# Kernel tuning notes

Measured on AMD Instinct MI355X. Metric: run time of the kernel, lower is better.

The kernel has to match this reference:

```python
import jax, jax.numpy as jnp
import numpy as np

B, DIMS = 8192, 1024
FCN = [DIMS, 2048, 1024, 512, 1]   # self.fcn_dims = [dims] + fcn_dims + [1]
C = 8                               # cluster_num
NLAYERS = len(FCN) - 1              # layer_num = 4


def setup_inputs() -> dict:
    key = jax.random.key(0)
    ks = jax.random.split(key, 2 + 2 * NLAYERS)
    inp = {}
    inp["x"] = jax.random.normal(ks[0], (B, DIMS), dtype=jnp.float32)
    # cluster centers, L2-normalized rows (as in __init__)
    c = jax.random.normal(ks[1], (C, DIMS), dtype=jnp.float32)
    inp["center"] = c / jnp.linalg.norm(c, axis=1, keepdims=True)
    for i in range(NLAYERS):
        fan_in, fan_out = FCN[i], FCN[i + 1]
        # xavier_uniform with relu gain
        gain = float(np.sqrt(2.0))
        bound = gain * float(np.sqrt(6.0 / (fan_in + fan_out)))
        inp[f"w0_{i}"] = jax.random.uniform(ks[2 + 2 * i], (fan_in, fan_out), jnp.float32, -bound, bound)
        inp[f"wc_{i}"] = jax.random.uniform(ks[3 + 2 * i], (C, fan_in, fan_out), jnp.float32, -bound, bound)
    return inp


def _forward(x, center, w0s, wcs):
    # --- router (eval mode: single pass, no center update, no grad) ---
    xd = jax.lax.stop_gradient(x)
    sij = xd @ jax.lax.stop_gradient(center).T          # [B, C]
    router = jnp.argmax(sij, axis=1)                     # [B]
    # --- all cluster towers, gated weights w0 * w_d ---
    h = jnp.broadcast_to(x[None], (C,) + x.shape)        # [C, B, dims]
    for i in range(NLAYERS - 1):
        w = w0s[i][None] * wcs[i]                        # [C, in, out]
        h = jax.nn.relu(jnp.einsum('cbi,cio->cbo', h, w))
    w = w0s[-1][None] * wcs[-1]                          # [C, in, 1]
    h = jax.nn.sigmoid(jnp.einsum('cbi,cio->cbo', h, w))  # [C, B, 1]
    out = jnp.transpose(h[:, :, 0])                      # [B, C]
    # gather per-sample selected cluster output
    return jnp.take_along_axis(out, router[:, None], axis=1)[:, 0]  # [B]


def reference(x, center, w0_0, w0_1, w0_2, w0_3, wc_0, wc_1, wc_2, wc_3):
    w0s = [w0_0, w0_1, w0_2, w0_3]
    wcs = [wc_0, wc_1, wc_2, wc_3]
    return _forward(x, center, w0s, wcs)
```

## Files before the change

kernel.cpp:

```cpp
#include <hip/hip_runtime.h>
#include <hip/hip_bf16.h>

#define B_SZ 8192
#define DIMS 1024
#define CLN 8
#define BM 128
#define PADMAX (B_SZ + CLN * BM)
#define MAX_TILES (B_SZ / BM + CLN)

typedef __attribute__((ext_vector_type(8))) __bf16 bf16x8;
typedef __attribute__((ext_vector_type(8))) short short8;
typedef __attribute__((ext_vector_type(4))) short short4v;
typedef __attribute__((ext_vector_type(4))) float f32x4;

__device__ __forceinline__ short f2bf(float f) {
  __hip_bfloat16 h = __float2bfloat16(f);
  return __builtin_bit_cast(short, h);
}
__device__ __forceinline__ float bf2f(short s) {
  unsigned u = ((unsigned)(unsigned short)s) << 16;
  return __builtin_bit_cast(float, u);
}

__device__ __forceinline__ void gl_lds16(const short* g, short* l) {
  __builtin_amdgcn_global_load_lds(
      (const __attribute__((address_space(1))) unsigned int*)(unsigned long long)(uintptr_t)g,
      (__attribute__((address_space(3))) unsigned int*)(unsigned long long)(uintptr_t)l,
      16, 0, 0);
}

__global__ void router_kernel(const float* __restrict__ x, const float* __restrict__ center,
                              int* __restrict__ router, short* __restrict__ xb) {
  const int tid = threadIdx.x;
  const int lane = tid & 63;
  const int w = tid >> 6;
  const int s = blockIdx.x * 4 + w;
  const float4* xr = (const float4*)(x + (size_t)s * DIMS);
  float4 xv[4];
#pragma unroll
  for (int j = 0; j < 4; ++j) xv[j] = xr[j * 64 + lane];
  if (xb) {
    short* xbr = xb + (size_t)s * DIMS;
#pragma unroll
    for (int j = 0; j < 4; ++j) {
      short4v sv;
      sv[0] = f2bf(xv[j].x); sv[1] = f2bf(xv[j].y);
      sv[2] = f2bf(xv[j].z); sv[3] = f2bf(xv[j].w);
      *(short4v*)(xbr + j * 256 + lane * 4) = sv;
    }
  }
  float p[CLN];
#pragma unroll
  for (int c = 0; c < CLN; ++c) {
    const float4* cr = (const float4*)(center + (size_t)c * DIMS);
    float acc = 0.f;
#pragma unroll
    for (int j = 0; j < 4; ++j) {
      float4 cv = cr[j * 64 + lane];
      acc += xv[j].x * cv.x + xv[j].y * cv.y + xv[j].z * cv.z + xv[j].w * cv.w;
    }
    p[c] = acc;
  }
#pragma unroll
  for (int c = 0; c < CLN; ++c) {
#pragma unroll
    for (int m = 1; m < 64; m <<= 1) p[c] += __shfl_xor(p[c], m);
  }
  if (lane == 0) {
    int best = 0; float bv = p[0];
#pragma unroll
    for (int c = 1; c < CLN; ++c) { if (p[c] > bv) { bv = p[c]; best = c; } }
    router[s] = best;
  }
}

__global__ void sort_kernel(const int* __restrict__ router, int* __restrict__ counts,
                            int* __restrict__ pstart, int* __restrict__ meta,
                            int* __restrict__ tile_c, int* __restrict__ tile_r,
                            int* __restrict__ order) {
  __shared__ int bins[CLN];
  __shared__ int cur[CLN];
  __shared__ int ps_s[CLN + 1];
  const int t = threadIdx.x;
  const int lane = t & 63;
  if (t < CLN) bins[t] = 0;
  __syncthreads();
  int myc[8];
#pragma unroll
  for (int j = 0; j < 8; ++j) myc[j] = router[t + 1024 * j];
#pragma unroll
  for (int j = 0; j < 8; ++j) {
#pragma unroll
    for (int c = 0; c < CLN; ++c) {
      unsigned long long m = __ballot(myc[j] == c);
      if (lane == 0 && m) atomicAdd(&bins[c], __popcll(m));
    }
  }
  __syncthreads();
  if (t == 0) {
    int ps = 0, nt = 0;
    for (int c = 0; c < CLN; ++c) {
      const int tot = bins[c];
      counts[c] = tot; pstart[c] = ps; ps_s[c] = ps; cur[c] = 0;
      const int tiles = (tot + BM - 1) / BM;
      for (int i = 0; i < tiles; ++i) { tile_c[nt] = c; tile_r[nt] = ps + i * BM; ++nt; }
      ps += tiles * BM;
    }
    pstart[CLN] = ps; ps_s[CLN] = ps; meta[0] = nt; meta[1] = ps;
  }
  __syncthreads();
#pragma unroll
  for (int j = 0; j < 8; ++j) {
    const int s = t + 1024 * j;
    const int c = myc[j];
    int pos = 0;
#pragma unroll
    for (int cc = 0; cc < CLN; ++cc) {
      unsigned long long m = __ballot(c == cc);
      int b = 0;
      if (lane == 0 && m) b = atomicAdd(&cur[cc], __popcll(m));
      b = __shfl(b, 0);
      if (c == cc) pos = ps_s[cc] + b + __popcll(m & ((1ull << lane) - 1ull));
    }
    order[pos] = s;
  }
  __syncthreads();
  for (int p = t; p < PADMAX; p += 1024) {
#pragma unroll
    for (int c = 0; c < CLN; ++c) {
      if (p >= ps_s[c] && p < ps_s[c + 1]) {
        if (p - ps_s[c] >= bins[c]) order[p] = order[ps_s[c]];
        break;
      }
    }
  }
}

template <int K, int N>
__device__ __forceinline__ void gate_body(const float* __restrict__ w0,
                                          const float* __restrict__ wc,
                                          short* __restrict__ gwt, int bx, short* t) {
  constexpr int NK = K / 32, NN = N / 64;
  const int c = bx / (NK * NN);
  const int rem = bx % (NK * NN);
  const int k0 = (rem % NK) * 32;
  const int n0 = (rem / NK) * 64;
  const int tid = threadIdx.x;
  const int lk = tid >> 4;
  const int ln = (tid & 15) * 4;
  const float* w0p = w0 + (size_t)k0 * N + n0;
  const float* wcp = wc + (size_t)c * K * N + (size_t)k0 * N + n0;
#pragma unroll
  for (int i = 0; i < 2; ++i) {
    const int k = lk + i * 16;
    float4 a = *(const float4*)(w0p + (size_t)k * N + ln);
    float4 b = *(const float4*)(wcp + (size_t)k * N + ln);
    short* d = &t[k * 65 + ln];
    d[0] = f2bf(a.x * b.x); d[1] = f2bf(a.y * b.y);
    d[2] = f2bf(a.z * b.z); d[3] = f2bf(a.w * b.w);
  }
  __syncthreads();
  const int wn = tid >> 2;
  const int wk = (tid & 3) * 8;
  short8 v;
#pragma unroll
  for (int j = 0; j < 8; ++j) v[j] = t[(wk + j) * 65 + wn];
  *(short8*)(gwt + ((size_t)c * N + n0 + wn) * K + k0 + wk) = v;
}

__global__ void gate_all(const float* __restrict__ w00, const float* __restrict__ wc0, short* g0,
                         const float* __restrict__ w01, const float* __restrict__ wc1, short* g1,
                         const float* __restrict__ w02, const float* __restrict__ wc2, short* g2) {
  __shared__ short t[32 * 65];
  const int bx = blockIdx.x;
  if (bx < 8192)       gate_body<1024, 2048>(w00, wc0, g0, bx, t);
  else if (bx < 16384) gate_body<2048, 1024>(w01, wc1, g1, bx - 8192, t);
  else                 gate_body<1024, 512>(w02, wc2, g2, bx - 16384, t);
}

template <int K, int N>
__global__ void gate_kernel(const float* __restrict__ w0, const float* __restrict__ wc,
                            short* __restrict__ gwt) {
  __shared__ short t[32 * 65];
  gate_body<K, N>(w0, wc, gwt, blockIdx.x, t);
}

template <int K, int N, bool GATHER>
__global__ void gemm_async(const short* __restrict__ Abase, const short* __restrict__ gwt,
                           short* __restrict__ Aout, const int* __restrict__ order,
                           const int* __restrict__ tile_c, const int* __restrict__ tile_r,
                           const int* __restrict__ meta) {
  constexpr int NT = N / 128;
  const int bt = blockIdx.x / NT;
  if (bt >= meta[0]) return;
  const int n0 = (blockIdx.x % NT) * 128;
  const int cl = tile_c[bt];
  const int row0 = tile_r[bt];

  __shared__ __align__(16) short As0[128 * 32];
  __shared__ __align__(16) short As1[128 * 32];
  __shared__ __align__(16) short Bs0[128 * 32];
  __shared__ __align__(16) short Bs1[128 * 32];

  const int tid = threadIdx.x;
  const int lane = tid & 63;
  const int w = tid >> 6;
  const int wm = w >> 1;
  const int wn = w & 1;

  const int lrow = lane >> 2;
  const int kofs = (lane & 3) << 3;
  const short* ga0;
  const short* ga1;
  if (GATHER) {
    ga0 = Abase + (size_t)order[row0 + w * 16 + lrow] * K + kofs;
    ga1 = Abase + (size_t)order[row0 + 64 + w * 16 + lrow] * K + kofs;
  } else {
    ga0 = Abase + (size_t)(row0 + w * 16 + lrow) * K + kofs;
    ga1 = ga0 + (size_t)64 * K;
  }
  const short* gb0 = gwt + ((size_t)cl * N + n0 + w * 16 + lrow) * K + kofs;
  const short* gb1 = gb0 + (size_t)64 * K;
  short* lo = (short*)((char*)nullptr);
  (void)lo;
  short* lA0a = &As0[w * 16 * 32];
  short* lA0b = &As0[(64 + w * 16) * 32];
  short* lA1a = &As1[w * 16 * 32];
  short* lA1b = &As1[(64 + w * 16) * 32];
  short* lB0a = &Bs0[w * 16 * 32];
  short* lB0b = &Bs0[(64 + w * 16) * 32];
  short* lB1a = &Bs1[w * 16 * 32];
  short* lB1b = &Bs1[(64 + w * 16) * 32];

  f32x4 acc[4][4] = {};
  const int arL = wm * 64 + (lane & 15);
  const int bcL = wn * 64 + (lane & 15);
  const int kq = (lane >> 4) << 3;

  for (int kb = 0; kb < K; kb += 64) {
    __syncthreads();
    gl_lds16(ga0 + kb, lA0a);
    gl_lds16(ga1 + kb, lA0b);
    gl_lds16(ga0 + kb + 32, lA1a);
    gl_lds16(ga1 + kb + 32, lA1b);
    gl_lds16(gb0 + kb, lB0a);
    gl_lds16(gb1 + kb, lB0b);
    gl_lds16(gb0 + kb + 32, lB1a);
    gl_lds16(gb1 + kb + 32, lB1b);
    __syncthreads();

#pragma unroll
    for (int h = 0; h < 2; ++h) {
      const short* Ap = h ? As1 : As0;
      const short* Bp = h ? Bs1 : Bs0;
      short8 af[4], bfr[4];
#pragma unroll
      for (int mi = 0; mi < 4; ++mi) af[mi] = *(const short8*)&Ap[(arL + mi * 16) * 32 + kq];
#pragma unroll
      for (int ni = 0; ni < 4; ++ni) bfr[ni] = *(const short8*)&Bp[(bcL + ni * 16) * 32 + kq];
#pragma unroll
      for (int mi = 0; mi < 4; ++mi) {
#pragma unroll
        for (int ni = 0; ni < 4; ++ni) {
          acc[mi][ni] = __builtin_amdgcn_mfma_f32_16x16x32_bf16(
              __builtin_bit_cast(bf16x8, af[mi]), __builtin_bit_cast(bf16x8, bfr[ni]),
              acc[mi][ni], 0, 0, 0);
        }
      }
    }
  }

  const int er = (lane >> 4) << 2;
  const int ec = lane & 15;
#pragma unroll
  for (int mi = 0; mi < 4; ++mi) {
#pragma unroll
    for (int ni = 0; ni < 4; ++ni) {
#pragma unroll
      for (int r = 0; r < 4; ++r) {
        float vv = fmaxf(acc[mi][ni][r], 0.f);
        const int row = row0 + wm * 64 + mi * 16 + er + r;
        const int col = n0 + wn * 64 + ni * 16 + ec;
        Aout[(size_t)row * N + col] = f2bf(vv);
      }
    }
  }
}

template <int K, int N, bool GATHER>
__global__ void gemm_layer(const float* __restrict__ Xf, const short* __restrict__ Ain,
                           const float* __restrict__ w0, const float* __restrict__ wc,
                           short* __restrict__ Aout,
                           const int* __restrict__ order,
                           const int* __restrict__ tile_c, const int* __restrict__ tile_r,
                           const int* __restrict__ meta) {
  const int bt = blockIdx.x;
  if (bt >= meta[0]) return;
  const int cl = tile_c[bt];
  const int row0 = tile_r[bt];
  const int n0 = blockIdx.y * 128;

  __shared__ __align__(16) short As[128 * 40];
  __shared__ __align__(16) short Bs[128 * 40];

  const int tid = threadIdx.x;
  const int lane = tid & 63;
  const int wm = (tid >> 6) >> 1;
  const int wn = (tid >> 6) & 1;

  f32x4 acc[4][4] = {};

  const int arow = tid >> 2;
  const int akseg = (tid & 3) << 3;
  const int bn = tid & 127;
  const int bkq = (tid >> 7) << 3;

  const float* xr0 = nullptr; const float* xr1 = nullptr;
  const short* ar0 = nullptr; const short* ar1 = nullptr;
  if (GATHER) {
    xr0 = Xf + (size_t)order[row0 + arow] * K + akseg;
    xr1 = Xf + (size_t)order[row0 + arow + 64] * K + akseg;
  } else {
    ar0 = Ain + (size_t)(row0 + arow) * K + akseg;
    ar1 = Ain + (size_t)(row0 + arow + 64) * K + akseg;
  }
  const float* w0p = w0 + n0 + bn;
  const float* wcp = wc + (size_t)cl * K * N + n0 + bn;

  for (int kb = 0; kb < K; kb += 32) {
    __syncthreads();
    if (GATHER) {
      float4 a = *(const float4*)(xr0 + kb);
      float4 b = *(const float4*)(xr0 + kb + 4);
      short8 v;
      v[0] = f2bf(a.x); v[1] = f2bf(a.y); v[2] = f2bf(a.z); v[3] = f2bf(a.w);
      v[4] = f2bf(b.x); v[5] = f2bf(b.y); v[6] = f2bf(b.z); v[7] = f2bf(b.w);
      *(short8*)&As[arow * 40 + akseg] = v;
      a = *(const float4*)(xr1 + kb);
      b = *(const float4*)(xr1 + kb + 4);
      v[0] = f2bf(a.x); v[1] = f2bf(a.y); v[2] = f2bf(a.z); v[3] = f2bf(a.w);
      v[4] = f2bf(b.x); v[5] = f2bf(b.y); v[6] = f2bf(b.z); v[7] = f2bf(b.w);
      *(short8*)&As[(arow + 64) * 40 + akseg] = v;
    } else {
      *(short8*)&As[arow * 40 + akseg] = *(const short8*)(ar0 + kb);
      *(short8*)&As[(arow + 64) * 40 + akseg] = *(const short8*)(ar1 + kb);
    }
#pragma unroll
    for (int half = 0; half < 2; ++half) {
      const int kk = bkq + half * 16;
      short8 v;
#pragma unroll
      for (int j = 0; j < 8; ++j) {
        const size_t off = (size_t)(kb + kk + j) * N;
        v[j] = f2bf(w0p[off] * wcp[off]);
      }
      *(short8*)&Bs[bn * 40 + kk] = v;
    }
    __syncthreads();

    const int arL = wm * 64 + (lane & 15);
    const int kq = (lane >> 4) << 3;
    const int bcL = wn * 64 + (lane & 15);
    short8 af[4], bfr[4];
#pragma unroll
    for (int mi = 0; mi < 4; ++mi) af[mi] = *(const short8*)&As[(arL + mi * 16) * 40 + kq];
#pragma unroll
    for (int ni = 0; ni < 4; ++ni) bfr[ni] = *(const short8*)&Bs[(bcL + ni * 16) * 40 + kq];
#pragma unroll
    for (int mi = 0; mi < 4; ++mi) {
#pragma unroll
      for (int ni = 0; ni < 4; ++ni) {
        acc[mi][ni] = __builtin_amdgcn_mfma_f32_16x16x32_bf16(
            __builtin_bit_cast(bf16x8, af[mi]), __builtin_bit_cast(bf16x8, bfr[ni]),
            acc[mi][ni], 0, 0, 0);
      }
    }
  }

  const int er = (lane >> 4) << 2;
  const int ec = lane & 15;
#pragma unroll
  for (int mi = 0; mi < 4; ++mi) {
#pragma unroll
    for (int ni = 0; ni < 4; ++ni) {
#pragma unroll
      for (int r = 0; r < 4; ++r) {
        float vv = fmaxf(acc[mi][ni][r], 0.f);
        const int row = row0 + wm * 64 + mi * 16 + er + r;
        const int col = n0 + wn * 64 + ni * 16 + ec;
        Aout[(size_t)row * N + col] = f2bf(vv);
      }
    }
  }
}

__global__ void layer3_kernel(const short* __restrict__ h2, const float* __restrict__ w03,
                              const float* __restrict__ wc3, const int* __restrict__ order,
                              const int* __restrict__ pstart, const int* __restrict__ meta,
                              float* __restrict__ out) {
  const int tid = threadIdx.x;
  const int lane = tid & 63;
  const int w = tid >> 6;
  const int r = blockIdx.x * 4 + w;
  if (r >= meta[1]) return;
  int c = 0;
#pragma unroll
  for (int i = 1; i < CLN; ++i) { if (r >= pstart[i]) c = i; }
  const short* hr = h2 + (size_t)r * 512;
  const int k0 = lane * 8;
  const short8 hv = *(const short8*)(hr + k0);
  const float* wcr = wc3 + c * 512;
  float part = 0.f;
#pragma unroll
  for (int j = 0; j < 8; ++j) part += bf2f(hv[j]) * w03[k0 + j] * wcr[k0 + j];
  for (int off = 32; off; off >>= 1) part += __shfl_down(part, off);
  if (lane == 0) out[order[r]] = 1.f / (1.f + expf(-part));
}

extern "C" void kernel_launch(void* const* d_in, const int* in_sizes, int n_in,
                              void* d_out, int out_size, void* d_ws, size_t ws_size,
                              hipStream_t stream) {
  const float* x = (const float*)d_in[0];
  const float* center = (const float*)d_in[1];
  const float* w0s[4]; const float* wcs[4];
  if (in_sizes[3] == 8 * in_sizes[2]) {
    for (int i = 0; i < 4; ++i) { w0s[i] = (const float*)d_in[2 + 2 * i]; wcs[i] = (const float*)d_in[3 + 2 * i]; }
  } else {
    for (int i = 0; i < 4; ++i) { w0s[i] = (const float*)d_in[2 + i]; wcs[i] = (const float*)d_in[6 + i]; }
  }
  float* out = (float*)d_out;
  char* ws = (char*)d_ws;
  int* counts = (int*)(ws + 0);
  int* pstart = (int*)(ws + 128);
  int* meta   = (int*)(ws + 192);
  int* tile_c = (int*)(ws + 256);
  int* tile_r = (int*)(ws + 1024);
  int* router = (int*)(ws + 4096);
  int* order  = (int*)(ws + 4096 + 4 * B_SZ);

  const size_t GW0 = (size_t)CLN * 1024 * 2048 * 2;
  const size_t GW1 = (size_t)CLN * 2048 * 1024 * 2;
  const size_t GW2 = (size_t)CLN * 1024 * 512 * 2;
  const size_t H0B = (size_t)PADMAX * 2048 * 2;
  const size_t H1B = (size_t)PADMAX * 1024 * 2;
  const size_t NEED_A = 131072 + GW0 + GW1 + GW2 + H0B + H1B;
  const size_t NEED_B = 131072 + GW1 + H0B + H1B;
  const int tier = (ws_size >= NEED_A) ? 0 : (ws_size >= NEED_B) ? 1 : 2;

  if (tier == 0) {
    short* gw0 = (short*)(ws + 131072);
    short* gw1 = (short*)(ws + 131072 + GW0);
    short* gw2 = (short*)(ws + 131072 + GW0 + GW1);
    short* h0  = (short*)(ws + 131072 + GW0 + GW1 + GW2);
    short* h1  = (short*)(ws + 131072 + GW0 + GW1 + GW2 + H0B);
    short* xb  = h1;
    short* h2  = h0;

    router_kernel<<<B_SZ / 4, 256, 0, stream>>>(x, center, router, xb);
    sort_kernel<<<1, 1024, 0, stream>>>(router, counts, pstart, meta, tile_c, tile_r, order);
    gate_all<<<18432, 256, 0, stream>>>(w0s[0], wcs[0], gw0, w0s[1], wcs[1], gw1,
                                        w0s[2], wcs[2], gw2);
    gemm_async<1024, 2048, true><<<MAX_TILES * 16, 256, 0, stream>>>(
        xb, gw0, h0, order, tile_c, tile_r, meta);
    gemm_async<2048, 1024, false><<<MAX_TILES * 8, 256, 0, stream>>>(
        h0, gw1, h1, order, tile_c, tile_r, meta);
    gemm_async<1024, 512, false><<<MAX_TILES * 4, 256, 0, stream>>>(
        h1, gw2, h2, order, tile_c, tile_r, meta);
    layer3_kernel<<<(PADMAX + 3) / 4, 256, 0, stream>>>(h2, w0s[3], wcs[3], order, pstart, meta, out);
  } else if (tier == 1) {
    short* gw = (short*)(ws + 131072);
    short* h0 = (short*)(ws + 131072 + GW1);
    short* h1 = (short*)(ws + 131072 + GW1 + H0B);
    short* xb = h1;
    short* h2 = h0;

    router_kernel<<<B_SZ / 4, 256, 0, stream>>>(x, center, router, xb);
    sort_kernel<<<1, 1024, 0, stream>>>(router, counts, pstart, meta, tile_c, tile_r, order);
    gate_kernel<1024, 2048><<<8192, 256, 0, stream>>>(w0s[0], wcs[0], gw);
    gemm_async<1024, 2048, true><<<MAX_TILES * 16, 256, 0, stream>>>(
        xb, gw, h0, order, tile_c, tile_r, meta);
    gate_kernel<2048, 1024><<<8192, 256, 0, stream>>>(w0s[1], wcs[1], gw);
    gemm_async<2048, 1024, false><<<MAX_TILES * 8, 256, 0, stream>>>(
        h0, gw, h1, order, tile_c, tile_r, meta);
    gate_kernel<1024, 512><<<2048, 256, 0, stream>>>(w0s[2], wcs[2], gw);
    gemm_async<1024, 512, false><<<MAX_TILES * 4, 256, 0, stream>>>(
        h1, gw, h2, order, tile_c, tile_r, meta);
    layer3_kernel<<<(PADMAX + 3) / 4, 256, 0, stream>>>(h2, w0s[3], wcs[3], order, pstart, meta, out);
  } else {
    short* f0 = (short*)(ws + 131072);
    short* f1 = f0 + (size_t)PADMAX * 2048;
    short* f2 = f1 + (size_t)PADMAX * 1024;
    router_kernel<<<B_SZ / 4, 256, 0, stream>>>(x, center, router, nullptr);
    sort_kernel<<<1, 1024, 0, stream>>>(router, counts, pstart, meta, tile_c, tile_r, order);
    gemm_layer<1024, 2048, true><<<dim3(MAX_TILES, 16), 256, 0, stream>>>(
        x, nullptr, w0s[0], wcs[0], f0, order, tile_c, tile_r, meta);
    gemm_layer<2048, 1024, false><<<dim3(MAX_TILES, 8), 256, 0, stream>>>(
        nullptr, f0, w0s[1], wcs[1], f1, order, tile_c, tile_r, meta);
    gemm_layer<1024, 512, false><<<dim3(MAX_TILES, 4), 256, 0, stream>>>(
        nullptr, f1, w0s[2], wcs[2], f2, order, tile_c, tile_r, meta);
    layer3_kernel<<<(PADMAX + 3) / 4, 256, 0, stream>>>(f2, w0s[3], wcs[3], order, pstart, meta, out);
  }
}
```

Baseline: 404.4 us.

## Fuse router with gating prep, fold final layer into GEMM epilogue, shrink K-step

Router and weight-gating work are merged into one prep kernel, and the gate transpose now uses 64x64 tiles with vectorised LDS writes. The last hidden layer's dot product with the gated output weights is fused into the third GEMM epilogue using shuffle reductions and atomicAdd into a z buffer that sort_kernel zeroes. A small final kernel applies the sigmoid and scatters results back to sample order. The GEMM main loop goes from a 64-wide K step with two LDS buffers to a 32-wide step with a single buffer, halving LDS use at the cost of twice as many barriers per K.

Result: faster. 396.2 us (-2.0%).

```diff
diff --git a/kernel.cpp b/kernel.cpp
--- a/kernel.cpp
+++ b/kernel.cpp
@@ -29,12 +29,14 @@
       16, 0, 0);
 }
 
-__global__ void router_kernel(const float* __restrict__ x, const float* __restrict__ center,
-                              int* __restrict__ router, short* __restrict__ xb) {
+__device__ __forceinline__ void router_body(const float* __restrict__ x,
+                                            const float* __restrict__ center,
+                                            int* __restrict__ router, short* __restrict__ xb,
+                                            int bx) {
   const int tid = threadIdx.x;
   const int lane = tid & 63;
   const int w = tid >> 6;
-  const int s = blockIdx.x * 4 + w;
+  const int s = bx * 4 + w;
   const float4* xr = (const float4*)(x + (size_t)s * DIMS);
   float4 xv[4];
 #pragma unroll
@@ -74,15 +76,89 @@
   }
 }
 
+#define GPAD 68
+template <int K, int N>
+__device__ __forceinline__ void gate_body(const float* __restrict__ w0,
+                                          const float* __restrict__ wc,
+                                          short* __restrict__ gwt, int bx, short* lds) {
+  constexpr int KB = K / 64, NB = N / 64;
+  const int c = bx / (KB * NB);
+  const int rem = bx % (KB * NB);
+  const int k0 = (rem % KB) * 64;
+  const int n0 = (rem / KB) * 64;
+  const int tid = threadIdx.x;
+  const int n4 = (tid & 15) * 4;
+  const int q = tid >> 4;
+  const float* w0p = w0 + (size_t)(k0 + q * 4) * N + n0 + n4;
+  const float* wcp = wc + ((size_t)c * K + k0 + q * 4) * N + n0 + n4;
+  float4 a[4], b[4];
+#pragma unroll
+  for (int j = 0; j < 4; ++j) {
+    a[j] = *(const float4*)(w0p + (size_t)j * N);
+    b[j] = *(const float4*)(wcp + (size_t)j * N);
+  }
+#pragma unroll
+  for (int jj = 0; jj < 4; ++jj) {
+    const float* af0 = (const float*)&a[0]; const float* bf0 = (const float*)&b[0];
+    const float* af1 = (const float*)&a[1]; const float* bf1 = (const float*)&b[1];
+    const float* af2 = (const float*)&a[2]; const float* bf2 = (const float*)&b[2];
+    const float* af3 = (const float*)&a[3]; const float* bf3 = (const float*)&b[3];
+    short4v sv;
+    sv[0] = f2bf(af0[jj] * bf0[jj]);
+    sv[1] = f2bf(af1[jj] * bf1[jj]);
+    sv[2] = f2bf(af2[jj] * bf2[jj]);
+    sv[3] = f2bf(af3[jj] * bf3[jj]);
+    *(short4v*)&lds[(n4 + jj) * GPAD + q * 4] = sv;
+  }
+  __syncthreads();
+  const int n = tid >> 2;
+  const int qg = tid & 3;
+  const short* src = &lds[n * GPAD + qg * 16];
+  short4v r0 = *(const short4v*)(src + 0);
+  short4v r1 = *(const short4v*)(src + 4);
+  short4v r2 = *(const short4v*)(src + 8);
+  short4v r3 = *(const short4v*)(src + 12);
+  short8 o0, o1;
+  o0[0]=r0[0]; o0[1]=r0[1]; o0[2]=r0[2]; o0[3]=r0[3];
+  o0[4]=r1[0]; o0[5]=r1[1]; o0[6]=r1[2]; o0[7]=r1[3];
+  o1[0]=r2[0]; o1[1]=r2[1]; o1[2]=r2[2]; o1[3]=r2[3];
+  o1[4]=r3[0]; o1[5]=r3[1]; o1[6]=r3[2]; o1[7]=r3[3];
+  short* dst = gwt + ((size_t)c * N + n0 + n) * K + k0 + qg * 16;
+  *(short8*)dst = o0;
+  *(short8*)(dst + 8) = o1;
+}
+
+__global__ void prep_kernel(const float* __restrict__ x, const float* __restrict__ center,
+                            int* __restrict__ router, short* __restrict__ xb,
+                            const float* w00, const float* wc0, short* g0,
+                            const float* w01, const float* wc1, short* g1,
+                            const float* w02, const float* wc2, short* g2) {
+  __shared__ short lds[64 * GPAD];
+  const int bx = blockIdx.x;
+  if (bx < 2048) { router_body(x, center, router, xb, bx); return; }
+  const int gx = bx - 2048;
+  if (gx < 4096)       gate_body<1024, 2048>(w00, wc0, g0, gx, lds);
+  else if (gx < 8192)  gate_body<2048, 1024>(w01, wc1, g1, gx - 4096, lds);
+  else                 gate_body<1024, 512>(w02, wc2, g2, gx - 8192, lds);
+}
+
+template <int K, int N>
+__global__ void gate1_kernel(const float* __restrict__ w0, const float* __restrict__ wc,
+                             short* __restrict__ gwt) {
+  __shared__ short lds[64 * GPAD];
+  gate_body<K, N>(w0, wc, gwt, blockIdx.x, lds);
+}
+
 __global__ void sort_kernel(const int* __restrict__ router, int* __restrict__ counts,
                             int* __restrict__ pstart, int* __restrict__ meta,
                             int* __restrict__ tile_c, int* __restrict__ tile_r,
-                            int* __restrict__ order) {
+                            int* __restrict__ order, float* __restrict__ z) {
   __shared__ int bins[CLN];
   __shared__ int cur[CLN];
   __shared__ int ps_s[CLN + 1];
   const int t = threadIdx.x;
   const int lane = t & 63;
+  for (int p = t; p < PADMAX; p += 1024) z[p] = 0.f;
   if (t < CLN) bins[t] = 0;
   __syncthreads();
   int myc[8];
@@ -136,60 +212,13 @@
   }
 }
 
-template <int K, int N>
-__device__ __forceinline__ void gate_body(const float* __restrict__ w0,
-                                          const float* __restrict__ wc,
-                                          short* __restrict__ gwt, int bx, short* t) {
-  constexpr int NK = K / 32, NN = N / 64;
-  const int c = bx / (NK * NN);
-  const int rem = bx % (NK * NN);
-  const int k0 = (rem % NK) * 32;
-  const int n0 = (rem / NK) * 64;
-  const int tid = threadIdx.x;
-  const int lk = tid >> 4;
-  const int ln = (tid & 15) * 4;
-  const float* w0p = w0 + (size_t)k0 * N + n0;
-  const float* wcp = wc + (size_t)c * K * N + (size_t)k0 * N + n0;
-#pragma unroll
-  for (int i = 0; i < 2; ++i) {
-    const int k = lk + i * 16;
-    float4 a = *(const float4*)(w0p + (size_t)k * N + ln);
-    float4 b = *(const float4*)(wcp + (size_t)k * N + ln);
-    short* d = &t[k * 65 + ln];
-    d[0] = f2bf(a.x * b.x); d[1] = f2bf(a.y * b.y);
-    d[2] = f2bf(a.z * b.z); d[3] = f2bf(a.w * b.w);
-  }
-  __syncthreads();
-  const int wn = tid >> 2;
-  const int wk = (tid & 3) * 8;
-  short8 v;
-#pragma unroll
-  for (int j = 0; j < 8; ++j) v[j] = t[(wk + j) * 65 + wn];
-  *(short8*)(gwt + ((size_t)c * N + n0 + wn) * K + k0 + wk) = v;
-}
-
-__global__ void gate_all(const float* __restrict__ w00, const float* __restrict__ wc0, short* g0,
-                         const float* __restrict__ w01, const float* __restrict__ wc1, short* g1,
-                         const float* __restrict__ w02, const float* __restrict__ wc2, short* g2) {
-  __shared__ short t[32 * 65];
-  const int bx = blockIdx.x;
-  if (bx < 8192)       gate_body<1024, 2048>(w00, wc0, g0, bx, t);
-  else if (bx < 16384) gate_body<2048, 1024>(w01, wc1, g1, bx - 8192, t);
-  else                 gate_body<1024, 512>(w02, wc2, g2, bx - 16384, t);
-}
-
-template <int K, int N>
-__global__ void gate_kernel(const float* __restrict__ w0, const float* __restrict__ wc,
-                            short* __restrict__ gwt) {
-  __shared__ short t[32 * 65];
-  gate_body<K, N>(w0, wc, gwt, blockIdx.x, t);
-}
-
-template <int K, int N, bool GATHER>
+template <int K, int N, bool GATHER, bool FUSE_DOT>
 __global__ void gemm_async(const short* __restrict__ Abase, const short* __restrict__ gwt,
                            short* __restrict__ Aout, const int* __restrict__ order,
                            const int* __restrict__ tile_c, const int* __restrict__ tile_r,
-                           const int* __restrict__ meta) {
+                           const int* __restrict__ meta,
+                           const float* __restrict__ w03, const float* __restrict__ wc3,
+                           float* __restrict__ z) {
   constexpr int NT = N / 128;
   const int bt = blockIdx.x / NT;
   if (bt >= meta[0]) return;
@@ -197,10 +226,8 @@
   const int cl = tile_c[bt];
   const int row0 = tile_r[bt];
 
-  __shared__ __align__(16) short As0[128 * 32];
-  __shared__ __align__(16) short As1[128 * 32];
-  __shared__ __align__(16) short Bs0[128 * 32];
-  __shared__ __align__(16) short Bs1[128 * 32];
+  __shared__ __align__(16) short As[128 * 32];
+  __shared__ __align__(16) short Bs[128 * 32];
 
   const int tid = threadIdx.x;
   const int lane = tid & 63;
@@ -221,70 +248,83 @@
   }
   const short* gb0 = gwt + ((size_t)cl * N + n0 + w * 16 + lrow) * K + kofs;
   const short* gb1 = gb0 + (size_t)64 * K;
-  short* lo = (short*)((char*)nullptr);
-  (void)lo;
-  short* lA0a = &As0[w * 16 * 32];
-  short* lA0b = &As0[(64 + w * 16) * 32];
-  short* lA1a = &As1[w * 16 * 32];
-  short* lA1b = &As1[(64 + w * 16) * 32];
-  short* lB0a = &Bs0[w * 16 * 32];
-  short* lB0b = &Bs0[(64 + w * 16) * 32];
-  short* lB1a = &Bs1[w * 16 * 32];
-  short* lB1b = &Bs1[(64 + w * 16) * 32];
+  short* lA0 = &As[w * 16 * 32];
+  short* lA1 = &As[(64 + w * 16) * 32];
+  short* lB0 = &Bs[w * 16 * 32];
+  short* lB1 = &Bs[(64 + w * 16) * 32];
 
   f32x4 acc[4][4] = {};
   const int arL = wm * 64 + (lane & 15);
   const int bcL = wn * 64 + (lane & 15);
   const int kq = (lane >> 4) << 3;
 
-  for (int kb = 0; kb < K; kb += 64) {
+  for (int kb = 0; kb < K; kb += 32) {
     __syncthreads();
-    gl_lds16(ga0 + kb, lA0a);
-    gl_lds16(ga1 + kb, lA0b);
-    gl_lds16(ga0 + kb + 32, lA1a);
-    gl_lds16(ga1 + kb + 32, lA1b);
-    gl_lds16(gb0 + kb, lB0a);
-    gl_lds16(gb1 + kb, lB0b);
-    gl_lds16(gb0 + kb + 32, lB1a);
-    gl_lds16(gb1 + kb + 32, lB1b);
+    gl_lds16(ga0 + kb, lA0);
+    gl_lds16(ga1 + kb, lA1);
+    gl_lds16(gb0 + kb, lB0);
+    gl_lds16(gb1 + kb, lB1);
     __syncthreads();
 
-#pragma unroll
-    for (int h = 0; h < 2; ++h) {
-      const short* Ap = h ? As1 : As0;
-      const short* Bp = h ? Bs1 : Bs0;
-      short8 af[4], bfr[4];
-#pragma unroll
-      for (int mi = 0; mi < 4; ++mi) af[mi] = *(const short8*)&Ap[(arL + mi * 16) * 32 + kq];
-#pragma unroll
-      for (int ni = 0; ni < 4; ++ni) bfr[ni] = *(const short8*)&Bp[(bcL + ni * 16) * 32 + kq];
-#pragma unroll
-      for (int mi = 0; mi < 4; ++mi) {
-#pragma unroll
-        for (int ni = 0; ni < 4; ++ni) {
-          acc[mi][ni] = __builtin_amdgcn_mfma_f32_16x16x32_bf16(
-              __builtin_bit_cast(bf16x8, af[mi]), __builtin_bit_cast(bf16x8, bfr[ni]),
-              acc[mi][ni], 0, 0, 0);
-        }
+    short8 af[4], bfr[4];
+#pragma unroll
+    for (int mi = 0; mi < 4; ++mi) af[mi] = *(const short8*)&As[(arL + mi * 16) * 32 + kq];
+#pragma unroll
+    for (int ni = 0; ni < 4; ++ni) bfr[ni] = *(const short8*)&Bs[(bcL + ni * 16) * 32 + kq];
+#pragma unroll
+    for (int mi = 0; mi < 4; ++mi) {
+#pragma unroll
+      for (int ni = 0; ni < 4; ++ni) {
+        acc[mi][ni] = __builtin_amdgcn_mfma_f32_16x16x32_bf16(
+            __builtin_bit_cast(bf16x8, af[mi]), __builtin_bit_cast(bf16x8, bfr[ni]),
+            acc[mi][ni], 0, 0, 0);
       }
     }
   }
 
   const int er = (lane >> 4) << 2;
   const int ec = lane & 15;
-#pragma unroll
-  for (int mi = 0; mi < 4; ++mi) {
+  if constexpr (FUSE_DOT) {
+    float g[4];
 #pragma unroll
     for (int ni = 0; ni < 4; ++ni) {
+      const int col = n0 + wn * 64 + ni * 16 + ec;
+      g[ni] = w03[col] * wc3[cl * N + col];
+    }
+#pragma unroll
+    for (int mi = 0; mi < 4; ++mi) {
 #pragma unroll
       for (int r = 0; r < 4; ++r) {
-        float vv = fmaxf(acc[mi][ni][r], 0.f);
-        const int row = row0 + wm * 64 + mi * 16 + er + r;
-        const int col = n0 + wn * 64 + ni * 16 + ec;
-        Aout[(size_t)row * N + col] = f2bf(vv);
-      }
-    }
-  }
+        float v = 0.f;
+#pragma unroll
+        for (int ni = 0; ni < 4; ++ni) v += fmaxf(acc[mi][ni][r], 0.f) * g[ni];
+#pragma unroll
+        for (int m = 1; m < 16; m <<= 1) v += __shfl_xor(v, m);
+        if ((lane & 15) == 0)
+          atomicAdd(&z[row0 + wm * 64 + mi * 16 + er + r], v);
+      }
+    }
+  } else {
+#pragma unroll
+    for (int mi = 0; mi < 4; ++mi) {
+#pragma unroll
+      for (int ni = 0; ni < 4; ++ni) {
+#pragma unroll
+        for (int r = 0; r < 4; ++r) {
+          float vv = fmaxf(acc[mi][ni][r], 0.f);
+          const int row = row0 + wm * 64 + mi * 16 + er + r;
+          const int col = n0 + wn * 64 + ni * 16 + ec;
+          Aout[(size_t)row * N + col] = f2bf(vv);
+        }
+      }
+    }
+  }
+}
+
+__global__ void final_kernel(const float* __restrict__ z, const int* __restrict__ order,
+                             const int* __restrict__ meta, float* __restrict__ out) {
+  const int r = blockIdx.x * 256 + threadIdx.x;
+  if (r < meta[1]) out[order[r]] = 1.f / (1.f + expf(-z[r]));
 }
 
 template <int K, int N, bool GATHER>
@@ -437,6 +477,7 @@
   int* tile_r = (int*)(ws + 1024);
   int* router = (int*)(ws + 4096);
   int* order  = (int*)(ws + 4096 + 4 * B_SZ);
+  float* z    = (float*)(ws + 4096 + 4 * B_SZ + 4 * PADMAX);
 
   const size_t GW0 = (size_t)CLN * 1024 * 2048 * 2;
   const size_t GW1 = (size_t)CLN * 2048 * 1024 * 2;
@@ -454,44 +495,47 @@
     short* h0  = (short*)(ws + 131072 + GW0 + GW1 + GW2);
     short* h1  = (short*)(ws + 131072 + GW0 + GW1 + GW2 + H0B);
     short* xb  = h1;
-    short* h2  = h0;
-
-    router_kernel<<<B_SZ / 4, 256, 0, stream>>>(x, center, router, xb);
-    sort_kernel<<<1, 1024, 0, stream>>>(router, counts, pstart, meta, tile_c, tile_r, order);
-    gate_all<<<18432, 256, 0, stream>>>(w0s[0], wcs[0], gw0, w0s[1], wcs[1], gw1,
-                                        w0s[2], wcs[2], gw2);
-    gemm_async<1024, 2048, true><<<MAX_TILES * 16, 256, 0, stream>>>(
-        xb, gw0, h0, order, tile_c, tile_r, meta);
-    gemm_async<2048, 1024, false><<<MAX_TILES * 8, 256, 0, stream>>>(
-        h0, gw1, h1, order, tile_c, tile_r, meta);
-    gemm_async<1024, 512, false><<<MAX_TILES * 4, 256, 0, stream>>>(
-        h1, gw2, h2, order, tile_c, tile_r, meta);
-    layer3_kernel<<<(PADMAX + 3) / 4, 256, 0, stream>>>(h2, w0s[3], wcs[3], order, pstart, meta, out);
+
+    prep_kernel<<<2048 + 9216, 256, 0, stream>>>(x, center, router, xb,
+                                                 w0s[0], wcs[0], gw0,
+                                                 w0s[1], wcs[1], gw1,
+                                                 w0s[2], wcs[2], gw2);
+    sort_kernel<<<1, 1024, 0, stream>>>(router, counts, pstart, meta, tile_c, tile_r, order, z);
+    gemm_async<1024, 2048, true, false><<<MAX_TILES * 16, 256, 0, stream>>>(
+        xb, gw0, h0, order, tile_c, tile_r, meta, nullptr, nullptr, nullptr);
+    gemm_async<2048, 1024, false, false><<<MAX_TILES * 8, 256, 0, stream>>>(
+        h0, gw1, h1, order, tile_c, tile_r, meta, nullptr, nullptr, nullptr);
+    gemm_async<1024, 512, false, true><<<MAX_TILES * 4, 256, 0, stream>>>(
+        h1, gw2, nullptr, order, tile_c, tile_r, meta, w0s[3], wcs[3], z);
+    final_kernel<<<PADMAX / 256, 256, 0, stream>>>(z, order, meta, out);
   } else if (tier == 1) {
     short* gw = (short*)(ws + 131072);
     short* h0 = (short*)(ws + 131072 + GW1);
     short* h1 = (short*)(ws + 131072 + GW1 + H0B);
     short* xb = h1;
-    short* h2 = h0;
-
-    router_kernel<<<B_SZ / 4, 256, 0, stream>>>(x, center, router, xb);
-    sort_kernel<<<1, 1024, 0, stream>>>(router, counts, pstart, meta, tile_c, tile_r, order);
-    gate_kernel<1024, 2048><<<8192, 256, 0, stream>>>(w0s[0], wcs[0], gw);
-    gemm_async<1024, 2048, true><<<MAX_TILES * 16, 256, 0, stream>>>(
-        xb, gw, h0, order, tile_c, tile_r, meta);
-    gate_kernel<2048, 1024><<<8192, 256, 0, stream>>>(w0s[1], wcs[1], gw);
-    gemm_async<2048, 1024, false><<<MAX_TILES * 8, 256, 0, stream>>>(
-        h0, gw, h1, order, tile_c, tile_r, meta);
-    gate_kernel<1024, 512><<<2048, 256, 0, stream>>>(w0s[2], wcs[2], gw);
-    gemm_async<1024, 512, false><<<MAX_TILES * 4, 256, 0, stream>>>(
-        h1, gw, h2, order, tile_c, tile_r, meta);
-    layer3_kernel<<<(PADMAX + 3) / 4, 256, 0, stream>>>(h2, w0s[3], wcs[3], order, pstart, meta, out);
+
+    prep_kernel<<<2048, 256, 0, stream>>>(x, center, router, xb,
+                                          nullptr, nullptr, nullptr, nullptr, nullptr,
+                                          nullptr, nullptr, nullptr, nullptr);
+    sort_kernel<<<1, 1024, 0, stream>>>(router, counts, pstart, meta, tile_c, tile_r, order, z);
+    gate1_kernel<1024, 2048><<<4096, 256, 0, stream>>>(w0s[0], wcs[0], gw);
+    gemm_async<1024, 2048, true, false><<<MAX_TILES * 16, 256, 0, stream>>>(
+        xb, gw, h0, order, tile_c, tile_r, meta, nullptr, nullptr, nullptr);
+    gate1_kernel<2048, 1024><<<4096, 256, 0, stream>>>(w0s[1], wcs[1], gw);
+    gemm_async<2048, 1024, false, false><<<MAX_TILES * 8, 256, 0, stream>>>(
+        h0, gw, h1, order, tile_c, tile_r, meta, nullptr, nullptr, nullptr);
+    gate1_kernel<1024, 512><<<1024, 256, 0, stream>>>(w0s[2], wcs[2], gw);
+    gemm_async<1024, 512, false, true><<<MAX_TILES * 4, 256, 0, stream>>>(
+        h1, gw, nullptr, order, tile_c, tile_r, meta, w0s[3], wcs[3], z);
+    final_kernel<<<PADMAX / 256, 256, 0, stream>>>(z, order, meta, out);
   } else {
     short* f0 = (short*)(ws + 131072);
     short* f1 = f0 + (size_t)PADMAX * 2048;
     short* f2 = f1 + (size_t)PADMAX * 1024;
-    router_kernel<<<B_SZ / 4, 256, 0, stream>>>(x, center, router, nullptr);
-    sort_kernel<<<1, 1024, 0, stream>>>(router, counts, pstart, meta, tile_c, tile_r, order);
+    prep_kernel<<<2048, 256, 0, stream>>>(x, center, router, nullptr,
+                                          nullptr, nullptr, nullptr, nullptr, nullptr,
+                                          nullptr, nullptr, nullptr, nullptr);
+    sort_kernel<<<1, 1024, 0, stream>>>(router, counts, pstart, meta, tile_c, tile_r, order, z);
     gemm_layer<1024, 2048, true><<<dim3(MAX_TILES, 16), 256, 0, stream>>>(
         x, nullptr, w0s[0], wcs[0], f0, order, tile_c, tile_r, meta);
     gemm_layer<2048, 1024, false><<<dim3(MAX_TILES, 8), 256, 0, stream>>>(
```
